# Performance work log

Measured on AMD Instinct MI355X. Metric: run time of the kernel, lower is better.

The kernel has to match this reference:

```python
import jax, jax.numpy as jnp
import numpy as np
from numpy.lib.stride_tricks import sliding_window_view

# Static configuration matching init_kwargs
F_, H_, W_ = 2, 32, 32          # video_shape
K = 5                            # kernel_size (odd)
HEADS, DIM_HEAD = 8, 64
N = F_ * H_ * W_                 # number of video tokens (2048)
PAD = K // 2
INNER = HEADS * DIM_HEAD         # 512


def _neighbors():
    # Flattened token index at each (f,h,w); pad with sentinel N (out of bounds -> zeros / masked)
    idx = np.arange(N, dtype=np.int32).reshape(F_, H_, W_)
    padded = np.full((F_ + 2 * PAD, H_ + 2 * PAD, W_ + 2 * PAD), N, dtype=np.int32)
    padded[PAD:PAD + F_, PAD:PAD + H_, PAD:PAD + W_] = idx
    # sliding_window_view matches unfoldNd's kernel-offset ordering (kf, kh, kw row-major)
    return sliding_window_view(padded, (K, K, K)).reshape(N, K ** 3)


NBR = jnp.asarray(_neighbors())                                   # [N, K^3]
# causal: query i attends only to neighbors with index <= i; prepend BOS column (never masked)
CAUSAL = jnp.pad(jnp.arange(N)[:, None] < NBR, ((0, 0), (1, 0)))  # [N, K^3 + 1]


def setup_inputs() -> dict:
    key = jax.random.key(0)
    k1, k2, k3 = jax.random.split(key, 3)
    return {
        "x": jax.random.normal(k1, (1, N, INNER), jnp.float32),
        "w_qkv": jax.random.normal(k2, (INNER, 3 * INNER), jnp.float32) * 0.02,
        "w_out": jax.random.normal(k3, (INNER, INNER), jnp.float32) * 0.02,
        "b_out": jnp.zeros((INNER,), jnp.float32),
    }


def reference(x, w_qkv, w_out, b_out):
    b, n, dim = x.shape            # n == N
    bh = b * HEADS
    scale = DIM_HEAD ** -0.5

    xp = jnp.pad(x, ((0, 0), (0, 1), (0, 0)))        # pad one zero token at the end: [b, n+1, dim]
    qkv = xp @ w_qkv                                  # [b, n+1, 3*inner]
    q, kk, vv = jnp.split(qkv, 3, axis=-1)

    def split_heads(t):  # 'b n (h d) -> (b h) n d'
        return t.reshape(b, n + 1, HEADS, DIM_HEAD).transpose(0, 2, 1, 3).reshape(bh, n + 1, DIM_HEAD)

    q, kk, vv = map(split_heads, (q, kk, vv))
    q = q[:, 1:] * scale                              # drop BOS query: [bh, n, d]
    k_bos, kk = kk[:, :1], kk[:, 1:]                  # BOS kv + n spatial tokens
    v_bos, vv = vv[:, :1], vv[:, 1:]

    # Append a zero row so the sentinel index N gathers zeros (== unfold's zero padding)
    zero = jnp.zeros((bh, 1, DIM_HEAD), kk.dtype)
    kw = jnp.concatenate([kk, zero], axis=1)[:, NBR]  # [bh, n, K^3, d]
    vw = jnp.concatenate([vv, zero], axis=1)[:, NBR]

    bos_k = jnp.broadcast_to(k_bos[:, None], (bh, n, 1, DIM_HEAD))
    bos_v = jnp.broadcast_to(v_bos[:, None], (bh, n, 1, DIM_HEAD))
    kw = jnp.concatenate([bos_k, kw], axis=2)         # [bh, n, K^3+1, d]
    vw = jnp.concatenate([bos_v, vw], axis=2)

    sim = jnp.einsum('bid,bijd->bij', q, kw)          # [bh, n, K^3+1]
    sim = jnp.where(CAUSAL[:n], -jnp.finfo(sim.dtype).max, sim)
    attn = jax.nn.softmax(sim, axis=-1)
    out = jnp.einsum('bij,bijd->bid', attn, vw)       # [bh, n, d]

    out = jnp.concatenate([v_bos, out], axis=1)       # BOS output = its value: [bh, n+1, d]
    out = out.reshape(b, HEADS, n + 1, DIM_HEAD).transpose(0, 2, 1, 3).reshape(b, n + 1, INNER)
    return (out @ w_out + b_out)[:, :n]
```

## Files before the change

### kernel.cpp

```cpp
#include <hip/hip_runtime.h>
#include <hip/hip_bf16.h>

#define NTOK  2048
#define INNER 512
#define KDIM  512
#define QKVP  1536

typedef __attribute__((ext_vector_type(8))) short bf16x8;
typedef __attribute__((ext_vector_type(4))) float f32x4;

__device__ __forceinline__ unsigned short f2b(float f) {
  unsigned int u = __float_as_uint(f);
  return (unsigned short)((u + 0x7FFFu + ((u >> 16) & 1u)) >> 16);
}

__device__ __forceinline__ void async_copy16(const unsigned short* g, unsigned short* l) {
  __builtin_amdgcn_global_load_lds((const __attribute__((address_space(1))) void*)g,
                                   (__attribute__((address_space(3))) void*)l, 16, 0, 0);
}

__global__ __launch_bounds__(256) void prep(const float* __restrict__ w_qkv,
                                            const float* __restrict__ w_out,
                                            unsigned short* __restrict__ wqkvT,
                                            unsigned short* __restrict__ woutT,
                                            int* __restrict__ glist,
                                            int* __restrict__ gcnt) {
  __shared__ float tile[32][33];
  __shared__ int list[192];
  __shared__ int cntS;
  const int tid = threadIdx.x;
  int b = blockIdx.x;

  if (b < 1024) {
    const float* in; unsigned short* out; int K, N, bx, by;
    if (b < 768) { in = w_qkv; out = wqkvT; K = 512; N = 1536; bx = b % 48; by = b / 48; }
    else { int bb = b - 768; in = w_out; out = woutT; K = 512; N = 512; bx = bb & 15; by = bb >> 4; }
    const int k0 = by * 32, n0 = bx * 32;
    const int r = tid >> 3, c4 = (tid & 7) * 4;
    float4 v = *(const float4*)(in + (size_t)(k0 + r) * N + n0 + c4);
    tile[r][c4 + 0] = v.x; tile[r][c4 + 1] = v.y;
    tile[r][c4 + 2] = v.z; tile[r][c4 + 3] = v.w;
    __syncthreads();
    ushort4 o;
    o.x = f2b(tile[c4 + 0][r]);
    o.y = f2b(tile[c4 + 1][r]);
    o.z = f2b(tile[c4 + 2][r]);
    o.w = f2b(tile[c4 + 3][r]);
    *(ushort4*)(out + (size_t)(n0 + r) * K + k0 + c4) = o;
    return;
  }

  const int pt = b - 1024;
  const int f  = pt >> 6;
  const int hh = (pt >> 1) & 31;
  const int w0 = (pt & 1) << 4;

  if (tid < 192) list[tid] = 0x7FFFFFFF;
  if (tid == 0) { list[0] = 0; cntS = 1; }
  __syncthreads();
  if (tid >= 1 && tid <= 160) {
    int cc = tid - 1;
    int p = cc / 20, wo = cc - p * 20;
    int ff = (p < 5) ? 0 : 1;
    int h2 = hh - 2 + ((p < 5) ? p : (p - 5));
    bool ok = (p < 5) ? ((f == 1) ? (h2 >= 0 && h2 <= 31) : (p <= 2 && h2 >= 0))
                      : (f == 1 && h2 >= 0);
    if (ok) {
      bool diag = (ff == f) && (h2 == hh);
      int wlo = max(0, w0 - 2);
      int whi = min(31, diag ? (w0 + 15) : (w0 + 17));
      int w2 = wlo + wo;
      if (w2 <= whi) {
        int pos = atomicAdd(&cntS, 1);
        list[pos] = ((ff << 10) | (h2 << 5) | w2) + 1;
      }
    }
  }
  __syncthreads();
  if (tid < 192) glist[pt * 192 + tid] = list[tid];
  if (tid == 0) gcnt[pt] = cntS;
}

__global__ __launch_bounds__(256, 2) void gemm_qkv(const float* __restrict__ x,
                                                   const unsigned short* __restrict__ Bt,
                                                   unsigned short* __restrict__ C) {
  constexpr int BK = 32, N = 1536, K = 512;
  __shared__ __align__(16) unsigned short As[64 * BK];
  __shared__ __align__(16) unsigned short Bs[128 * BK];
  const int tid = threadIdx.x, lane = tid & 63, wave = tid >> 6;
  const int m0 = blockIdx.y * 64, n0 = blockIdx.x * 128;
  const int wm = (wave >> 1) * 32, wn = (wave & 1) * 64;
  const int ar = tid >> 2, ac = (tid & 3) * 8;
  const int bl0 = ((wave * 2 + 0) * 64 + lane) * 8;
  const int bl1 = ((wave * 2 + 1) * 64 + lane) * 8;
  const int bn0 = bl0 >> 5, bk0 = bl0 & 31;
  const int bn1 = bl1 >> 5, bk1 = bl1 & 31;
  const int fr = lane & 15, fk = (lane >> 4) * 8;

  f32x4 acc[2][4] = {};

  for (int k0 = 0; k0 < K; k0 += BK) {
    async_copy16(Bt + (size_t)(n0 + bn0) * K + k0 + bk0, &Bs[bl0]);
    async_copy16(Bt + (size_t)(n0 + bn1) * K + k0 + bk1, &Bs[bl1]);
    const float* ap = x + (size_t)(m0 + ar) * K + k0 + ac;
    float4 a0 = *(const float4*)(ap);
    float4 a1 = *(const float4*)(ap + 4);
    bf16x8 av;
    av[0] = (short)f2b(a0.x); av[1] = (short)f2b(a0.y);
    av[2] = (short)f2b(a0.z); av[3] = (short)f2b(a0.w);
    av[4] = (short)f2b(a1.x); av[5] = (short)f2b(a1.y);
    av[6] = (short)f2b(a1.z); av[7] = (short)f2b(a1.w);
    *(bf16x8*)&As[ar * BK + ac] = av;
    __syncthreads();

    bf16x8 af[2], bfr[4];
#pragma unroll
    for (int i = 0; i < 2; ++i) af[i] = *(const bf16x8*)&As[(wm + i * 16 + fr) * BK + fk];
#pragma unroll
    for (int j = 0; j < 4; ++j) bfr[j] = *(const bf16x8*)&Bs[(wn + j * 16 + fr) * BK + fk];
#pragma unroll
    for (int i = 0; i < 2; ++i)
#pragma unroll
      for (int j = 0; j < 4; ++j)
        acc[i][j] = __builtin_amdgcn_mfma_f32_16x16x32_bf16(af[i], bfr[j], acc[i][j], 0, 0, 0);
    __syncthreads();
  }

  const int er = (lane >> 4) * 4, ec = lane & 15;
#pragma unroll
  for (int i = 0; i < 2; ++i)
#pragma unroll
    for (int j = 0; j < 4; ++j) {
      const int col = n0 + wn + j * 16 + ec;
#pragma unroll
      for (int r = 0; r < 4; ++r) {
        const int row = m0 + wm + i * 16 + er + r;
        C[(size_t)row * N + col] = f2b(acc[i][j][r]);
      }
    }
}

__global__ __launch_bounds__(256, 2) void gemm_out(const unsigned short* __restrict__ A,
                                                   const unsigned short* __restrict__ Bt,
                                                   const float* __restrict__ bias,
                                                   float* __restrict__ C) {
  constexpr int BK = 32, N = 512, K = 512;
  __shared__ __align__(16) unsigned short As[64 * BK];
  __shared__ __align__(16) unsigned short Bs[64 * BK];
  const int tid = threadIdx.x, lane = tid & 63, wave = tid >> 6;
  const int m0 = blockIdx.y * 64, n0 = blockIdx.x * 64;
  const int wm = (wave >> 1) * 32, wn = (wave & 1) * 32;
  const int li = tid * 8, r = li >> 5, c = li & 31;
  const int fr = lane & 15, fk = (lane >> 4) * 8;

  f32x4 acc[2][2] = {};

  for (int k0 = 0; k0 < K; k0 += BK) {
    async_copy16(A  + (size_t)(m0 + r) * K + k0 + c, &As[li]);
    async_copy16(Bt + (size_t)(n0 + r) * K + k0 + c, &Bs[li]);
    __syncthreads();
    bf16x8 af[2], bfr[2];
#pragma unroll
    for (int i = 0; i < 2; ++i) af[i] = *(const bf16x8*)&As[(wm + i * 16 + fr) * BK + fk];
#pragma unroll
    for (int j = 0; j < 2; ++j) bfr[j] = *(const bf16x8*)&Bs[(wn + j * 16 + fr) * BK + fk];
#pragma unroll
    for (int i = 0; i < 2; ++i)
#pragma unroll
      for (int j = 0; j < 2; ++j)
        acc[i][j] = __builtin_amdgcn_mfma_f32_16x16x32_bf16(af[i], bfr[j], acc[i][j], 0, 0, 0);
    __syncthreads();
  }

  const int er = (lane >> 4) * 4, ec = lane & 15;
#pragma unroll
  for (int i = 0; i < 2; ++i)
#pragma unroll
    for (int j = 0; j < 2; ++j) {
      const int col = n0 + wn + j * 16 + ec;
      const float b = bias[col];
#pragma unroll
      for (int rr = 0; rr < 4; ++rr) {
        const int row = m0 + wm + i * 16 + er + rr;
        C[(size_t)row * N + col] = acc[i][j][rr] + b;
      }
    }
}

__global__ __launch_bounds__(256) void attn_mfma(const unsigned short* __restrict__ qkv,
                                                 const int* __restrict__ glist,
                                                 const int* __restrict__ gcnt,
                                                 unsigned short* __restrict__ O) {
  __shared__ __align__(16) int list[192];
  __shared__ __align__(16) float mOd[2][16][72];
  __shared__ float mM[2][16], mL[2][16];
  __shared__ int cntS;

  const int tid = threadIdx.x;
  const int hp = blockIdx.y;

  if (blockIdx.x == 128) {
    if (tid < 128) O[hp * 128 + tid] = qkv[1024 + hp * 128 + tid];
    return;
  }
  const int pt = blockIdx.x;
  const int f  = pt >> 6;
  const int hh = (pt >> 1) & 31;
  const int w0 = (pt & 1) << 4;
  const int base_i = (f << 10) | (hh << 5) | w0;

  if (tid < 192) list[tid] = glist[pt * 192 + tid];
  if (tid == 0) cntS = gcnt[pt];
  __syncthreads();
  const int cnt  = cntS;
  const int nsub = (cnt + 15) >> 4;

  const int lane = tid & 63;
  const int wave = tid >> 6;
  const int hw   = wave >> 1;
  const int half = wave & 1;
  const int head = hp * 2 + hw;
  const int quad = lane >> 4;
  const int ec   = lane & 15;

  const int i_q = base_i + ec;
  const int tq  = min(i_q + 1, 2047);
  const unsigned short* qrow = qkv + (size_t)tq * QKVP + head * 64 + quad * 8;
  const bf16x8 qb0 = *(const bf16x8*)(qrow);
  const bf16x8 qb1 = *(const bf16x8*)(qrow + 32);

  f32x4 Od[4] = {{0,0,0,0},{0,0,0,0},{0,0,0,0},{0,0,0,0}};
  float m = -1e30f, l = 0.0f;

  for (int sub = half; sub < nsub; sub += 2) {
    const int base = sub * 16;
    const int tok_e = list[base + ec];
    const int4 tokv = *(const int4*)&list[base + quad * 4];
    const int tk[4] = {tokv.x, tokv.y, tokv.z, tokv.w};

    f32x4 S = {0, 0, 0, 0};
    {
      const int t0 = (tok_e > 2047) ? 0 : tok_e;
      const unsigned short* kr = qkv + (size_t)t0 * QKVP + 512 + head * 64 + quad * 8;
      const bf16x8 kf0 = *(const bf16x8*)(kr);
      const bf16x8 kf1 = *(const bf16x8*)(kr + 32);
      S = __builtin_amdgcn_mfma_f32_16x16x32_bf16(kf0, qb0, S, 0, 0, 0);
      S = __builtin_amdgcn_mfma_f32_16x16x32_bf16(kf1, qb1, S, 0, 0, 0);
    }

    float Sm[4];
#pragma unroll
    for (int r = 0; r < 4; ++r) {
      const int tok = tk[r];
      const int idx = tok - 1;
      const bool v = (tok == 0) ||
                     ((idx <= i_q) && ((unsigned)((idx & 31) - (w0 + ec) + 2) <= 4u));
      Sm[r] = v ? S[r] * 0.125f : -1e30f;
    }
    float mx = fmaxf(fmaxf(Sm[0], Sm[1]), fmaxf(Sm[2], Sm[3]));
    mx = fmaxf(mx, __shfl_xor(mx, 16, 64));
    mx = fmaxf(mx, __shfl_xor(mx, 32, 64));
    const float mn = fmaxf(m, mx);
    const float corr = __expf(m - mn);
    m = mn;
    const float p0 = __expf(Sm[0] - mn);
    const float p1 = __expf(Sm[1] - mn);
    const float p2 = __expf(Sm[2] - mn);
    const float p3 = __expf(Sm[3] - mn);
    float rs = (p0 + p1) + (p2 + p3);
    rs += __shfl_xor(rs, 16, 64);
    rs += __shfl_xor(rs, 32, 64);
    l = l * corr + rs;

    bf16x8 pf;
    pf[0] = (short)f2b(p0); pf[1] = (short)f2b(p1);
    pf[2] = (short)f2b(p2); pf[3] = (short)f2b(p3);
    pf[4] = 0; pf[5] = 0; pf[6] = 0; pf[7] = 0;

    const unsigned short* vp[4];
#pragma unroll
    for (int j = 0; j < 4; ++j) {
      const int tv = (tk[j] > 2047) ? 0 : tk[j];
      vp[j] = qkv + (size_t)tv * QKVP + 1024 + head * 64 + ec;
    }
#pragma unroll
    for (int dt = 0; dt < 4; ++dt) {
      bf16x8 vf;
#pragma unroll
      for (int j = 0; j < 4; ++j) vf[j] = (short)vp[j][dt * 16];
      vf[4] = 0; vf[5] = 0; vf[6] = 0; vf[7] = 0;
#pragma unroll
      for (int r = 0; r < 4; ++r) Od[dt][r] *= corr;
      Od[dt] = __builtin_amdgcn_mfma_f32_16x16x32_bf16(vf, pf, Od[dt], 0, 0, 0);
    }
  }

  if (half == 1) {
#pragma unroll
    for (int dt = 0; dt < 4; ++dt)
      *(f32x4*)&mOd[hw][ec][dt * 16 + quad * 4] = Od[dt];
    if (quad == 0) { mM[hw][ec] = m; mL[hw][ec] = l; }
  }
  __syncthreads();
  if (half == 0 && i_q <= 2046) {
    const float m1 = mM[hw][ec], l1 = mL[hw][ec];
    const float mm = fmaxf(m, m1);
    const float c0 = __expf(m - mm), c1 = __expf(m1 - mm);
    const float rl = 1.0f / (l * c0 + l1 * c1);
    unsigned short* ob = O + (size_t)(i_q + 1) * 512 + head * 64 + quad * 4;
#pragma unroll
    for (int dt = 0; dt < 4; ++dt) {
      const f32x4 o1 = *(const f32x4*)&mOd[hw][ec][dt * 16 + quad * 4];
      ushort4 u;
      u.x = f2b((Od[dt][0] * c0 + o1[0] * c1) * rl);
      u.y = f2b((Od[dt][1] * c0 + o1[1] * c1) * rl);
      u.z = f2b((Od[dt][2] * c0 + o1[2] * c1) * rl);
      u.w = f2b((Od[dt][3] * c0 + o1[3] * c1) * rl);
      *(ushort4*)(ob + dt * 16) = u;
    }
  }
}


extern "C" void kernel_launch(void* const* d_in, const int* in_sizes, int n_in,
                              void* d_out, int out_size, void* d_ws, size_t ws_size,
                              hipStream_t stream) {
  const float* x     = (const float*)d_in[0];
  const float* w_qkv = (const float*)d_in[1];
  const float* w_out = (const float*)d_in[2];
  const float* b_out = (const float*)d_in[3];
  float* out = (float*)d_out;

  char* ws = (char*)d_ws;
  unsigned short* qkvb  = (unsigned short*)(ws);
  unsigned short* wqkvT = (unsigned short*)(ws + 6291456);
  unsigned short* woutT = (unsigned short*)(ws + 7864320);
  unsigned short* Ob    = (unsigned short*)(ws + 8388608);
  int*            glist = (int*)(ws + 10485760);
  int*            gcnt  = (int*)(ws + 10584064);

  hipLaunchKernelGGL(prep, dim3(1152), dim3(256), 0, stream,
                     w_qkv, w_out, wqkvT, woutT, glist, gcnt);

  hipLaunchKernelGGL(gemm_qkv, dim3(12, 32), dim3(256), 0, stream, x, wqkvT, qkvb);

  hipLaunchKernelGGL(attn_mfma, dim3(129, 4), dim3(256), 0, stream, qkvb, glist, gcnt, Ob);

  hipLaunchKernelGGL(gemm_out, dim3(8, 32), dim3(256), 0, stream, Ob, woutT, b_out, out);
}
```

Baseline: 99.36 us.

## Fuse neighborhood attention with output projection and build neighbor lists in-kernel

Attention and the output GEMM are merged into one kernel. Each 512-thread block handles 16 query tokens across all 8 heads (one wave per head), stages the bf16 attention output in LDS, and multiplies it by the output weights with MFMA. Neighbor-list construction moves from the prep kernel into the attention block, which removes the global list buffers and the intermediate O buffer. The split-KV halves and their merge step are dropped. In exchange the grid shrinks from 516 to 129 blocks, each wave walks all KV subtiles serially, and W_out is read from global memory by every block.

```diff
diff --git a/kernel.cpp b/kernel.cpp
--- a/kernel.cpp
+++ b/kernel.cpp
@@ -13,6 +13,9 @@
   unsigned int u = __float_as_uint(f);
   return (unsigned short)((u + 0x7FFFu + ((u >> 16) & 1u)) >> 16);
 }
+__device__ __forceinline__ float b2f(unsigned short u) {
+  return __uint_as_float(((unsigned int)u) << 16);
+}
 
 __device__ __forceinline__ void async_copy16(const unsigned short* g, unsigned short* l) {
   __builtin_amdgcn_global_load_lds((const __attribute__((address_space(1))) void*)g,
@@ -22,38 +25,121 @@
 __global__ __launch_bounds__(256) void prep(const float* __restrict__ w_qkv,
                                             const float* __restrict__ w_out,
                                             unsigned short* __restrict__ wqkvT,
-                                            unsigned short* __restrict__ woutT,
-                                            int* __restrict__ glist,
-                                            int* __restrict__ gcnt) {
+                                            unsigned short* __restrict__ woutT) {
   __shared__ float tile[32][33];
-  __shared__ int list[192];
-  __shared__ int cntS;
   const int tid = threadIdx.x;
   int b = blockIdx.x;
-
-  if (b < 1024) {
-    const float* in; unsigned short* out; int K, N, bx, by;
-    if (b < 768) { in = w_qkv; out = wqkvT; K = 512; N = 1536; bx = b % 48; by = b / 48; }
-    else { int bb = b - 768; in = w_out; out = woutT; K = 512; N = 512; bx = bb & 15; by = bb >> 4; }
-    const int k0 = by * 32, n0 = bx * 32;
-    const int r = tid >> 3, c4 = (tid & 7) * 4;
-    float4 v = *(const float4*)(in + (size_t)(k0 + r) * N + n0 + c4);
-    tile[r][c4 + 0] = v.x; tile[r][c4 + 1] = v.y;
-    tile[r][c4 + 2] = v.z; tile[r][c4 + 3] = v.w;
+  const float* in; unsigned short* out; int K, N, bx, by;
+  if (b < 768) { in = w_qkv; out = wqkvT; K = 512; N = 1536; bx = b % 48; by = b / 48; }
+  else { int bb = b - 768; in = w_out; out = woutT; K = 512; N = 512; bx = bb & 15; by = bb >> 4; }
+  const int k0 = by * 32, n0 = bx * 32;
+  const int r = tid >> 3, c4 = (tid & 7) * 4;
+  float4 v = *(const float4*)(in + (size_t)(k0 + r) * N + n0 + c4);
+  tile[r][c4 + 0] = v.x; tile[r][c4 + 1] = v.y;
+  tile[r][c4 + 2] = v.z; tile[r][c4 + 3] = v.w;
+  __syncthreads();
+  ushort4 o;
+  o.x = f2b(tile[c4 + 0][r]);
+  o.y = f2b(tile[c4 + 1][r]);
+  o.z = f2b(tile[c4 + 2][r]);
+  o.w = f2b(tile[c4 + 3][r]);
+  *(ushort4*)(out + (size_t)(n0 + r) * K + k0 + c4) = o;
+}
+
+__global__ __launch_bounds__(256, 2) void gemm_qkv(const float* __restrict__ x,
+                                                   const unsigned short* __restrict__ Bt,
+                                                   unsigned short* __restrict__ C) {
+  constexpr int BK = 32, N = 1536, K = 512;
+  __shared__ __align__(16) unsigned short As[64 * BK];
+  __shared__ __align__(16) unsigned short Bs[128 * BK];
+  const int tid = threadIdx.x, lane = tid & 63, wave = tid >> 6;
+  const int m0 = blockIdx.y * 64, n0 = blockIdx.x * 128;
+  const int wm = (wave >> 1) * 32, wn = (wave & 1) * 64;
+  const int ar = tid >> 2, ac = (tid & 3) * 8;
+  const int bl0 = ((wave * 2 + 0) * 64 + lane) * 8;
+  const int bl1 = ((wave * 2 + 1) * 64 + lane) * 8;
+  const int bn0 = bl0 >> 5, bk0 = bl0 & 31;
+  const int bn1 = bl1 >> 5, bk1 = bl1 & 31;
+  const int fr = lane & 15, fk = (lane >> 4) * 8;
+
+  f32x4 acc[2][4] = {};
+
+  for (int k0 = 0; k0 < K; k0 += BK) {
+    async_copy16(Bt + (size_t)(n0 + bn0) * K + k0 + bk0, &Bs[bl0]);
+    async_copy16(Bt + (size_t)(n0 + bn1) * K + k0 + bk1, &Bs[bl1]);
+    const float* ap = x + (size_t)(m0 + ar) * K + k0 + ac;
+    float4 a0 = *(const float4*)(ap);
+    float4 a1 = *(const float4*)(ap + 4);
+    bf16x8 av;
+    av[0] = (short)f2b(a0.x); av[1] = (short)f2b(a0.y);
+    av[2] = (short)f2b(a0.z); av[3] = (short)f2b(a0.w);
+    av[4] = (short)f2b(a1.x); av[5] = (short)f2b(a1.y);
+    av[6] = (short)f2b(a1.z); av[7] = (short)f2b(a1.w);
+    *(bf16x8*)&As[ar * BK + ac] = av;
     __syncthreads();
-    ushort4 o;
-    o.x = f2b(tile[c4 + 0][r]);
-    o.y = f2b(tile[c4 + 1][r]);
-    o.z = f2b(tile[c4 + 2][r]);
-    o.w = f2b(tile[c4 + 3][r]);
-    *(ushort4*)(out + (size_t)(n0 + r) * K + k0 + c4) = o;
+
+    bf16x8 af[2], bfr[4];
+#pragma unroll
+    for (int i = 0; i < 2; ++i) af[i] = *(const bf16x8*)&As[(wm + i * 16 + fr) * BK + fk];
+#pragma unroll
+    for (int j = 0; j < 4; ++j) bfr[j] = *(const bf16x8*)&Bs[(wn + j * 16 + fr) * BK + fk];
+#pragma unroll
+    for (int i = 0; i < 2; ++i)
+#pragma unroll
+      for (int j = 0; j < 4; ++j)
+        acc[i][j] = __builtin_amdgcn_mfma_f32_16x16x32_bf16(af[i], bfr[j], acc[i][j], 0, 0, 0);
+    __syncthreads();
+  }
+
+  const int er = (lane >> 4) * 4, ec = lane & 15;
+#pragma unroll
+  for (int i = 0; i < 2; ++i)
+#pragma unroll
+    for (int j = 0; j < 4; ++j) {
+      const int col = n0 + wn + j * 16 + ec;
+#pragma unroll
+      for (int r = 0; r < 4; ++r) {
+        const int row = m0 + wm + i * 16 + er + r;
+        C[(size_t)row * N + col] = f2b(acc[i][j][r]);
+      }
+    }
+}
+
+__global__ __launch_bounds__(512) void attn_out(const unsigned short* __restrict__ qkv,
+                                                const unsigned short* __restrict__ woutT,
+                                                const float* __restrict__ bias,
+                                                float* __restrict__ out) {
+  __shared__ __align__(16) int list[192];
+  __shared__ int cntS;
+  __shared__ __align__(16) unsigned short Osh[16][520];
+
+  const int tid  = threadIdx.x;
+  const int lane = tid & 63;
+  const int wave = tid >> 6;
+  const int quad = lane >> 4;
+  const int ec   = lane & 15;
+
+  if (blockIdx.x == 128) {
+    __shared__ unsigned short V0[512];
+    V0[tid] = qkv[1024 + tid];
+    __syncthreads();
+    const unsigned short* wr = woutT + (size_t)tid * 512;
+    float acc = 0.0f;
+#pragma unroll 4
+    for (int k = 0; k < 512; k += 8) {
+      bf16x8 wv = *(const bf16x8*)(wr + k);
+#pragma unroll
+      for (int j = 0; j < 8; ++j) acc += b2f(V0[k + j]) * b2f((unsigned short)wv[j]);
+    }
+    out[tid] = acc + bias[tid];
     return;
   }
 
-  const int pt = b - 1024;
+  const int pt = blockIdx.x;
   const int f  = pt >> 6;
   const int hh = (pt >> 1) & 31;
   const int w0 = (pt & 1) << 4;
+  const int base_i = (f << 10) | (hh << 5) | w0;
 
   if (tid < 192) list[tid] = 0x7FFFFFFF;
   if (tid == 0) { list[0] = 0; cntS = 1; }
@@ -77,152 +163,9 @@
     }
   }
   __syncthreads();
-  if (tid < 192) glist[pt * 192 + tid] = list[tid];
-  if (tid == 0) gcnt[pt] = cntS;
-}
-
-__global__ __launch_bounds__(256, 2) void gemm_qkv(const float* __restrict__ x,
-                                                   const unsigned short* __restrict__ Bt,
-                                                   unsigned short* __restrict__ C) {
-  constexpr int BK = 32, N = 1536, K = 512;
-  __shared__ __align__(16) unsigned short As[64 * BK];
-  __shared__ __align__(16) unsigned short Bs[128 * BK];
-  const int tid = threadIdx.x, lane = tid & 63, wave = tid >> 6;
-  const int m0 = blockIdx.y * 64, n0 = blockIdx.x * 128;
-  const int wm = (wave >> 1) * 32, wn = (wave & 1) * 64;
-  const int ar = tid >> 2, ac = (tid & 3) * 8;
-  const int bl0 = ((wave * 2 + 0) * 64 + lane) * 8;
-  const int bl1 = ((wave * 2 + 1) * 64 + lane) * 8;
-  const int bn0 = bl0 >> 5, bk0 = bl0 & 31;
-  const int bn1 = bl1 >> 5, bk1 = bl1 & 31;
-  const int fr = lane & 15, fk = (lane >> 4) * 8;
-
-  f32x4 acc[2][4] = {};
-
-  for (int k0 = 0; k0 < K; k0 += BK) {
-    async_copy16(Bt + (size_t)(n0 + bn0) * K + k0 + bk0, &Bs[bl0]);
-    async_copy16(Bt + (size_t)(n0 + bn1) * K + k0 + bk1, &Bs[bl1]);
-    const float* ap = x + (size_t)(m0 + ar) * K + k0 + ac;
-    float4 a0 = *(const float4*)(ap);
-    float4 a1 = *(const float4*)(ap + 4);
-    bf16x8 av;
-    av[0] = (short)f2b(a0.x); av[1] = (short)f2b(a0.y);
-    av[2] = (short)f2b(a0.z); av[3] = (short)f2b(a0.w);
-    av[4] = (short)f2b(a1.x); av[5] = (short)f2b(a1.y);
-    av[6] = (short)f2b(a1.z); av[7] = (short)f2b(a1.w);
-    *(bf16x8*)&As[ar * BK + ac] = av;
-    __syncthreads();
-
-    bf16x8 af[2], bfr[4];
-#pragma unroll
-    for (int i = 0; i < 2; ++i) af[i] = *(const bf16x8*)&As[(wm + i * 16 + fr) * BK + fk];
-#pragma unroll
-    for (int j = 0; j < 4; ++j) bfr[j] = *(const bf16x8*)&Bs[(wn + j * 16 + fr) * BK + fk];
-#pragma unroll
-    for (int i = 0; i < 2; ++i)
-#pragma unroll
-      for (int j = 0; j < 4; ++j)
-        acc[i][j] = __builtin_amdgcn_mfma_f32_16x16x32_bf16(af[i], bfr[j], acc[i][j], 0, 0, 0);
-    __syncthreads();
-  }
-
-  const int er = (lane >> 4) * 4, ec = lane & 15;
-#pragma unroll
-  for (int i = 0; i < 2; ++i)
-#pragma unroll
-    for (int j = 0; j < 4; ++j) {
-      const int col = n0 + wn + j * 16 + ec;
-#pragma unroll
-      for (int r = 0; r < 4; ++r) {
-        const int row = m0 + wm + i * 16 + er + r;
-        C[(size_t)row * N + col] = f2b(acc[i][j][r]);
-      }
-    }
-}
-
-__global__ __launch_bounds__(256, 2) void gemm_out(const unsigned short* __restrict__ A,
-                                                   const unsigned short* __restrict__ Bt,
-                                                   const float* __restrict__ bias,
-                                                   float* __restrict__ C) {
-  constexpr int BK = 32, N = 512, K = 512;
-  __shared__ __align__(16) unsigned short As[64 * BK];
-  __shared__ __align__(16) unsigned short Bs[64 * BK];
-  const int tid = threadIdx.x, lane = tid & 63, wave = tid >> 6;
-  const int m0 = blockIdx.y * 64, n0 = blockIdx.x * 64;
-  const int wm = (wave >> 1) * 32, wn = (wave & 1) * 32;
-  const int li = tid * 8, r = li >> 5, c = li & 31;
-  const int fr = lane & 15, fk = (lane >> 4) * 8;
-
-  f32x4 acc[2][2] = {};
-
-  for (int k0 = 0; k0 < K; k0 += BK) {
-    async_copy16(A  + (size_t)(m0 + r) * K + k0 + c, &As[li]);
-    async_copy16(Bt + (size_t)(n0 + r) * K + k0 + c, &Bs[li]);
-    __syncthreads();
-    bf16x8 af[2], bfr[2];
-#pragma unroll
-    for (int i = 0; i < 2; ++i) af[i] = *(const bf16x8*)&As[(wm + i * 16 + fr) * BK + fk];
-#pragma unroll
-    for (int j = 0; j < 2; ++j) bfr[j] = *(const bf16x8*)&Bs[(wn + j * 16 + fr) * BK + fk];
-#pragma unroll
-    for (int i = 0; i < 2; ++i)
-#pragma unroll
-      for (int j = 0; j < 2; ++j)
-        acc[i][j] = __builtin_amdgcn_mfma_f32_16x16x32_bf16(af[i], bfr[j], acc[i][j], 0, 0, 0);
-    __syncthreads();
-  }
-
-  const int er = (lane >> 4) * 4, ec = lane & 15;
-#pragma unroll
-  for (int i = 0; i < 2; ++i)
-#pragma unroll
-    for (int j = 0; j < 2; ++j) {
-      const int col = n0 + wn + j * 16 + ec;
-      const float b = bias[col];
-#pragma unroll
-      for (int rr = 0; rr < 4; ++rr) {
-        const int row = m0 + wm + i * 16 + er + rr;
-        C[(size_t)row * N + col] = acc[i][j][rr] + b;
-      }
-    }
-}
-
-__global__ __launch_bounds__(256) void attn_mfma(const unsigned short* __restrict__ qkv,
-                                                 const int* __restrict__ glist,
-                                                 const int* __restrict__ gcnt,
-                                                 unsigned short* __restrict__ O) {
-  __shared__ __align__(16) int list[192];
-  __shared__ __align__(16) float mOd[2][16][72];
-  __shared__ float mM[2][16], mL[2][16];
-  __shared__ int cntS;
-
-  const int tid = threadIdx.x;
-  const int hp = blockIdx.y;
-
-  if (blockIdx.x == 128) {
-    if (tid < 128) O[hp * 128 + tid] = qkv[1024 + hp * 128 + tid];
-    return;
-  }
-  const int pt = blockIdx.x;
-  const int f  = pt >> 6;
-  const int hh = (pt >> 1) & 31;
-  const int w0 = (pt & 1) << 4;
-  const int base_i = (f << 10) | (hh << 5) | w0;
-
-  if (tid < 192) list[tid] = glist[pt * 192 + tid];
-  if (tid == 0) cntS = gcnt[pt];
-  __syncthreads();
-  const int cnt  = cntS;
-  const int nsub = (cnt + 15) >> 4;
-
-  const int lane = tid & 63;
-  const int wave = tid >> 6;
-  const int hw   = wave >> 1;
-  const int half = wave & 1;
-  const int head = hp * 2 + hw;
-  const int quad = lane >> 4;
-  const int ec   = lane & 15;
-
+  const int nsub = (cntS + 15) >> 4;
+
+  const int head = wave;
   const int i_q = base_i + ec;
   const int tq  = min(i_q + 1, 2047);
   const unsigned short* qrow = qkv + (size_t)tq * QKVP + head * 64 + quad * 8;
@@ -232,7 +175,7 @@
   f32x4 Od[4] = {{0,0,0,0},{0,0,0,0},{0,0,0,0},{0,0,0,0}};
   float m = -1e30f, l = 0.0f;
 
-  for (int sub = half; sub < nsub; sub += 2) {
+  for (int sub = 0; sub < nsub; ++sub) {
     const int base = sub * 16;
     const int tok_e = list[base + ec];
     const int4 tokv = *(const int4*)&list[base + quad * 4];
@@ -295,28 +238,44 @@
     }
   }
 
-  if (half == 1) {
-#pragma unroll
-    for (int dt = 0; dt < 4; ++dt)
-      *(f32x4*)&mOd[hw][ec][dt * 16 + quad * 4] = Od[dt];
-    if (quad == 0) { mM[hw][ec] = m; mL[hw][ec] = l; }
+  {
+    const float rl = 1.0f / l;
+#pragma unroll
+    for (int dt = 0; dt < 4; ++dt) {
+      ushort4 u;
+      u.x = f2b(Od[dt][0] * rl);
+      u.y = f2b(Od[dt][1] * rl);
+      u.z = f2b(Od[dt][2] * rl);
+      u.w = f2b(Od[dt][3] * rl);
+      *(ushort4*)&Osh[ec][head * 64 + dt * 16 + quad * 4] = u;
+    }
   }
   __syncthreads();
-  if (half == 0 && i_q <= 2046) {
-    const float m1 = mM[hw][ec], l1 = mL[hw][ec];
-    const float mm = fmaxf(m, m1);
-    const float c0 = __expf(m - mm), c1 = __expf(m1 - mm);
-    const float rl = 1.0f / (l * c0 + l1 * c1);
-    unsigned short* ob = O + (size_t)(i_q + 1) * 512 + head * 64 + quad * 4;
-#pragma unroll
-    for (int dt = 0; dt < 4; ++dt) {
-      const f32x4 o1 = *(const f32x4*)&mOd[hw][ec][dt * 16 + quad * 4];
-      ushort4 u;
-      u.x = f2b((Od[dt][0] * c0 + o1[0] * c1) * rl);
-      u.y = f2b((Od[dt][1] * c0 + o1[1] * c1) * rl);
-      u.z = f2b((Od[dt][2] * c0 + o1[2] * c1) * rl);
-      u.w = f2b((Od[dt][3] * c0 + o1[3] * c1) * rl);
-      *(ushort4*)(ob + dt * 16) = u;
+
+  const int fr = lane & 15, fk = quad * 8;
+  const int nb = wave * 64;
+  f32x4 accD[4] = {{0,0,0,0},{0,0,0,0},{0,0,0,0},{0,0,0,0}};
+#pragma unroll
+  for (int k0 = 0; k0 < 512; k0 += 32) {
+    const bf16x8 af = *(const bf16x8*)&Osh[fr][k0 + fk];
+    bf16x8 bfr[4];
+#pragma unroll
+    for (int j = 0; j < 4; ++j)
+      bfr[j] = *(const bf16x8*)(woutT + (size_t)(nb + j * 16 + fr) * 512 + k0 + fk);
+#pragma unroll
+    for (int j = 0; j < 4; ++j)
+      accD[j] = __builtin_amdgcn_mfma_f32_16x16x32_bf16(af, bfr[j], accD[j], 0, 0, 0);
+  }
+
+  const int er = quad * 4;
+#pragma unroll
+  for (int j = 0; j < 4; ++j) {
+    const int col = nb + j * 16 + ec;
+    const float b = bias[col];
+#pragma unroll
+    for (int r = 0; r < 4; ++r) {
+      const int t = base_i + 1 + er + r;
+      if (t <= 2047) out[(size_t)t * 512 + col] = accD[j][r] + b;
     }
   }
 }
@@ -335,16 +294,10 @@
   unsigned short* qkvb  = (unsigned short*)(ws);
   unsigned short* wqkvT = (unsigned short*)(ws + 6291456);
   unsigned short* woutT = (unsigned short*)(ws + 7864320);
-  unsigned short* Ob    = (unsigned short*)(ws + 8388608);
-  int*            glist = (int*)(ws + 10485760);
-  int*            gcnt  = (int*)(ws + 10584064);
-
-  hipLaunchKernelGGL(prep, dim3(1152), dim3(256), 0, stream,
-                     w_qkv, w_out, wqkvT, woutT, glist, gcnt);
+
+  hipLaunchKernelGGL(prep, dim3(1024), dim3(256), 0, stream, w_qkv, w_out, wqkvT, woutT);
 
   hipLaunchKernelGGL(gemm_qkv, dim3(12, 32), dim3(256), 0, stream, x, wqkvT, qkvb);
 
-  hipLaunchKernelGGL(attn_mfma, dim3(129, 4), dim3(256), 0, stream, qkvb, glist, gcnt, Ob);
-
-  hipLaunchKernelGGL(gemm_out, dim3(8, 32), dim3(256), 0, stream, Ob, woutT, b_out, out);
-}
+  hipLaunchKernelGGL(attn_out, dim3(129), dim3(512), 0, stream, qkvb, woutT, b_out, out);
+}
```

Result: slower. 110.4 us (+11.1%).

## Pre-convert x to bf16 in prep and shrink GEMM tiles for more blocks

Applied to the files above, without the earlier changes.

Moves the fp32-to-bf16 conversion of x into extra blocks of the prep kernel, so gemm_qkv can load A tiles with async global-to-LDS copies instead of converting inline. gemm_qkv switches to 64x64 tiles (24x32 grid), and gemm_out to 32x64 tiles (8x64 grid), both with higher occupancy hints. The aim is more blocks to fill the CUs and less conversion work in the GEMM inner loop. The cost is an extra bf16 copy of x written and reread through memory, plus less data reuse per tile.

```diff
diff --git a/kernel.cpp b/kernel.cpp
--- a/kernel.cpp
+++ b/kernel.cpp
@@ -21,8 +21,10 @@
 
 __global__ __launch_bounds__(256) void prep(const float* __restrict__ w_qkv,
                                             const float* __restrict__ w_out,
+                                            const float* __restrict__ x,
                                             unsigned short* __restrict__ wqkvT,
                                             unsigned short* __restrict__ woutT,
+                                            unsigned short* __restrict__ xb,
                                             int* __restrict__ glist,
                                             int* __restrict__ gcnt) {
   __shared__ float tile[32][33];
@@ -30,6 +32,15 @@
   __shared__ int cntS;
   const int tid = threadIdx.x;
   int b = blockIdx.x;
+
+  if (b >= 1152) {
+    const int i = (b - 1152) * 1024 + tid * 4;
+    float4 v = *(const float4*)(x + i);
+    ushort4 o;
+    o.x = f2b(v.x); o.y = f2b(v.y); o.z = f2b(v.z); o.w = f2b(v.w);
+    *(ushort4*)(xb + i) = o;
+    return;
+  }
 
   if (b < 1024) {
     const float* in; unsigned short* out; int K, N, bx, by;
@@ -81,70 +92,10 @@
   if (tid == 0) gcnt[pt] = cntS;
 }
 
-__global__ __launch_bounds__(256, 2) void gemm_qkv(const float* __restrict__ x,
+__global__ __launch_bounds__(256, 4) void gemm_qkv(const unsigned short* __restrict__ A,
                                                    const unsigned short* __restrict__ Bt,
                                                    unsigned short* __restrict__ C) {
   constexpr int BK = 32, N = 1536, K = 512;
-  __shared__ __align__(16) unsigned short As[64 * BK];
-  __shared__ __align__(16) unsigned short Bs[128 * BK];
-  const int tid = threadIdx.x, lane = tid & 63, wave = tid >> 6;
-  const int m0 = blockIdx.y * 64, n0 = blockIdx.x * 128;
-  const int wm = (wave >> 1) * 32, wn = (wave & 1) * 64;
-  const int ar = tid >> 2, ac = (tid & 3) * 8;
-  const int bl0 = ((wave * 2 + 0) * 64 + lane) * 8;
-  const int bl1 = ((wave * 2 + 1) * 64 + lane) * 8;
-  const int bn0 = bl0 >> 5, bk0 = bl0 & 31;
-  const int bn1 = bl1 >> 5, bk1 = bl1 & 31;
-  const int fr = lane & 15, fk = (lane >> 4) * 8;
-
-  f32x4 acc[2][4] = {};
-
-  for (int k0 = 0; k0 < K; k0 += BK) {
-    async_copy16(Bt + (size_t)(n0 + bn0) * K + k0 + bk0, &Bs[bl0]);
-    async_copy16(Bt + (size_t)(n0 + bn1) * K + k0 + bk1, &Bs[bl1]);
-    const float* ap = x + (size_t)(m0 + ar) * K + k0 + ac;
-    float4 a0 = *(const float4*)(ap);
-    float4 a1 = *(const float4*)(ap + 4);
-    bf16x8 av;
-    av[0] = (short)f2b(a0.x); av[1] = (short)f2b(a0.y);
-    av[2] = (short)f2b(a0.z); av[3] = (short)f2b(a0.w);
-    av[4] = (short)f2b(a1.x); av[5] = (short)f2b(a1.y);
-    av[6] = (short)f2b(a1.z); av[7] = (short)f2b(a1.w);
-    *(bf16x8*)&As[ar * BK + ac] = av;
-    __syncthreads();
-
-    bf16x8 af[2], bfr[4];
-#pragma unroll
-    for (int i = 0; i < 2; ++i) af[i] = *(const bf16x8*)&As[(wm + i * 16 + fr) * BK + fk];
-#pragma unroll
-    for (int j = 0; j < 4; ++j) bfr[j] = *(const bf16x8*)&Bs[(wn + j * 16 + fr) * BK + fk];
-#pragma unroll
-    for (int i = 0; i < 2; ++i)
-#pragma unroll
-      for (int j = 0; j < 4; ++j)
-        acc[i][j] = __builtin_amdgcn_mfma_f32_16x16x32_bf16(af[i], bfr[j], acc[i][j], 0, 0, 0);
-    __syncthreads();
-  }
-
-  const int er = (lane >> 4) * 4, ec = lane & 15;
-#pragma unroll
-  for (int i = 0; i < 2; ++i)
-#pragma unroll
-    for (int j = 0; j < 4; ++j) {
-      const int col = n0 + wn + j * 16 + ec;
-#pragma unroll
-      for (int r = 0; r < 4; ++r) {
-        const int row = m0 + wm + i * 16 + er + r;
-        C[(size_t)row * N + col] = f2b(acc[i][j][r]);
-      }
-    }
-}
-
-__global__ __launch_bounds__(256, 2) void gemm_out(const unsigned short* __restrict__ A,
-                                                   const unsigned short* __restrict__ Bt,
-                                                   const float* __restrict__ bias,
-                                                   float* __restrict__ C) {
-  constexpr int BK = 32, N = 512, K = 512;
   __shared__ __align__(16) unsigned short As[64 * BK];
   __shared__ __align__(16) unsigned short Bs[64 * BK];
   const int tid = threadIdx.x, lane = tid & 63, wave = tid >> 6;
@@ -178,13 +129,54 @@
 #pragma unroll
     for (int j = 0; j < 2; ++j) {
       const int col = n0 + wn + j * 16 + ec;
-      const float b = bias[col];
 #pragma unroll
       for (int rr = 0; rr < 4; ++rr) {
         const int row = m0 + wm + i * 16 + er + rr;
-        C[(size_t)row * N + col] = acc[i][j][rr] + b;
+        C[(size_t)row * N + col] = f2b(acc[i][j][rr]);
       }
     }
+}
+
+__global__ __launch_bounds__(256, 4) void gemm_out(const unsigned short* __restrict__ A,
+                                                   const unsigned short* __restrict__ Bt,
+                                                   const float* __restrict__ bias,
+                                                   float* __restrict__ C) {
+  constexpr int BK = 32, N = 512, K = 512;
+  __shared__ __align__(16) unsigned short As[32 * BK];
+  __shared__ __align__(16) unsigned short Bs[64 * BK];
+  const int tid = threadIdx.x, lane = tid & 63, wave = tid >> 6;
+  const int m0 = blockIdx.y * 32, n0 = blockIdx.x * 64;
+  const int wm = (wave >> 1) * 16, wn = (wave & 1) * 32;
+  const int li = tid * 8, r = li >> 5, c = li & 31;
+  const int fr = lane & 15, fk = (lane >> 4) * 8;
+
+  f32x4 acc[2] = {};
+
+  for (int k0 = 0; k0 < K; k0 += BK) {
+    if (tid < 128) async_copy16(A + (size_t)(m0 + r) * K + k0 + c, &As[li]);
+    async_copy16(Bt + (size_t)(n0 + r) * K + k0 + c, &Bs[li]);
+    __syncthreads();
+    bf16x8 af, bfr[2];
+    af = *(const bf16x8*)&As[(wm + fr) * BK + fk];
+#pragma unroll
+    for (int j = 0; j < 2; ++j) bfr[j] = *(const bf16x8*)&Bs[(wn + j * 16 + fr) * BK + fk];
+#pragma unroll
+    for (int j = 0; j < 2; ++j)
+      acc[j] = __builtin_amdgcn_mfma_f32_16x16x32_bf16(af, bfr[j], acc[j], 0, 0, 0);
+    __syncthreads();
+  }
+
+  const int er = (lane >> 4) * 4, ec = lane & 15;
+#pragma unroll
+  for (int j = 0; j < 2; ++j) {
+    const int col = n0 + wn + j * 16 + ec;
+    const float b = bias[col];
+#pragma unroll
+    for (int rr = 0; rr < 4; ++rr) {
+      const int row = m0 + wm + er + rr;
+      C[(size_t)row * N + col] = acc[j][rr] + b;
+    }
+  }
 }
 
 __global__ __launch_bounds__(256) void attn_mfma(const unsigned short* __restrict__ qkv,
@@ -212,8 +204,7 @@
   if (tid < 192) list[tid] = glist[pt * 192 + tid];
   if (tid == 0) cntS = gcnt[pt];
   __syncthreads();
-  const int cnt  = cntS;
-  const int nsub = (cnt + 15) >> 4;
+  const int nsub = (cntS + 15) >> 4;
 
   const int lane = tid & 63;
   const int wave = tid >> 6;
@@ -336,15 +327,16 @@
   unsigned short* wqkvT = (unsigned short*)(ws + 6291456);
   unsigned short* woutT = (unsigned short*)(ws + 7864320);
   unsigned short* Ob    = (unsigned short*)(ws + 8388608);
-  int*            glist = (int*)(ws + 10485760);
-  int*            gcnt  = (int*)(ws + 10584064);
-
-  hipLaunchKernelGGL(prep, dim3(1152), dim3(256), 0, stream,
-                     w_qkv, w_out, wqkvT, woutT, glist, gcnt);
-
-  hipLaunchKernelGGL(gemm_qkv, dim3(12, 32), dim3(256), 0, stream, x, wqkvT, qkvb);
+  unsigned short* xb    = (unsigned short*)(ws + 10485760);
+  int*            glist = (int*)(ws + 12582912);
+  int*            gcnt  = (int*)(ws + 12681216);
+
+  hipLaunchKernelGGL(prep, dim3(2176), dim3(256), 0, stream,
+                     w_qkv, w_out, x, wqkvT, woutT, xb, glist, gcnt);
+
+  hipLaunchKernelGGL(gemm_qkv, dim3(24, 32), dim3(256), 0, stream, xb, wqkvT, qkvb);
 
   hipLaunchKernelGGL(attn_mfma, dim3(129, 4), dim3(256), 0, stream, qkvb, glist, gcnt, Ob);
 
-  hipLaunchKernelGGL(gemm_out, dim3(8, 32), dim3(256), 0, stream, Ob, woutT, b_out, out);
-}
+  hipLaunchKernelGGL(gemm_out, dim3(8, 64), dim3(256), 0, stream, Ob, woutT, b_out, out);
+}
```

Result: faster. 96.29 us, median of 2 (-3.1%).
